# Kernel optimization log

Measured on AMD Instinct MI355X. Metric: run time of the kernel, lower is better.

## Reference

```python
import jax, jax.numpy as jnp
import numpy as np

B, R, NB, T = 32, 96, 5, 2048
FEAT_DIM = 64
SPARSITY = 0.2


def _per_band(X, community, W1, b1, W2, b2):
    # X: [R, T] wavelet coeffs for one (batch, band) slice
    n, t = X.shape
    f32 = X.dtype
    # --- functional connectivity (cosine of centered signals == Pearson corr) ---
    Xc = X - X.mean(axis=1, keepdims=True)
    norm = jnp.linalg.norm(Xc, axis=1, keepdims=True)
    norm = jnp.where(norm == 0, 1.0, norm)
    C = (Xc @ Xc.T) / (norm * norm.T)
    C = jnp.nan_to_num(C, nan=0.0)
    C = C * (1.0 - jnp.eye(n, dtype=f32))  # zero diagonal
    # --- quantile sparsification over strict lower triangle ---
    ti, tj = np.tril_indices(n, -1)
    thr = jnp.quantile(jnp.abs(C[ti, tj]), 1.0 - SPARSITY)
    A = C * (jnp.abs(C) >= thr).astype(f32)  # graph_type == 'weighted'
    # --- node features (5-dim, averaged over regions) ---
    mean_f = X.mean(axis=1)
    std_f = jnp.std(X, axis=1, ddof=1)  # torch.std is unbiased
    energy_f = (X ** 2).sum(axis=1)
    maxamp_f = jnp.abs(X).max(axis=1)
    ps = jnp.abs(jnp.fft.fft(X, axis=1)) ** 2
    ps = ps[:, : t // 2]
    s = ps.sum(axis=1, keepdims=True)
    s = jnp.where(s == 0, 1.0, s)
    p = ps / s
    ent_f = -(p * jnp.log(p + 1e-10)).sum(axis=1)
    node5 = jnp.stack([mean_f, std_f, energy_f, maxamp_f, ent_f], axis=1).mean(axis=0)
    # --- graph properties (6-dim) on binarized adjacency ---
    Bm = (A != 0).astype(f32)
    ne = Bm.sum() / 2.0
    density = ne / (n * (n - 1) / 2.0)
    deg = Bm.sum(axis=1)
    avg_deg = deg.mean()
    A2 = Bm @ Bm
    tri = (A2 * Bm).sum() / 6.0
    poss = (deg * (deg - 1.0)).sum() / 2.0
    clus = jnp.where(poss > 0, tri / jnp.where(poss > 0, poss, 1.0), 0.0)
    # global efficiency: safe reciprocal (zero where A+I == 0; original would emit inf)
    denom = Bm + jnp.eye(n, dtype=f32)
    eff = jnp.where(denom > 0, 1.0 / jnp.where(denom > 0, denom, 1.0), 0.0).sum() / (n * (n - 1))
    # approximate modularity with fixed 2-community assignment (deterministic)
    m2 = 2.0 * ne
    m2_safe = jnp.where(m2 > 0, m2, 1.0)
    same = (community[:, None] == community[None, :]) & (~jnp.eye(n, dtype=bool))
    expected = jnp.outer(deg, deg) / m2_safe
    mod = jnp.where(m2 > 0, (same * (Bm - expected)).sum() / m2_safe, 0.0)
    props = jnp.stack([ne, density, avg_deg, clus, eff, mod])
    feat11 = jnp.concatenate([node5, props])  # [11]
    # --- feature encoder MLP (dropout is identity at inference) ---
    h = jnp.maximum(feat11 @ W1.T + b1, 0.0)
    return A, h @ W2.T + b2


def _forward(wavelet_coeffs, frequency_bands, community, W1, b1, W2, b2):
    b, r, nb, t = wavelet_coeffs.shape
    Xs = wavelet_coeffs.transpose(0, 2, 1, 3).reshape(b * nb, r, t)  # [B*NB, R, T]
    A, F = jax.vmap(_per_band, in_axes=(0, None, None, None, None, None))(
        Xs, community, W1, b1, W2, b2)
    return A.reshape(b, nb, r, r), F.reshape(b, nb, -1)


def setup_inputs() -> dict:
    key = jax.random.key(0)
    k0, k1, k2, k3, k4 = jax.random.split(key, 5)
    wavelet_coeffs = jax.random.normal(k0, (B, R, NB, T), dtype=jnp.float32)
    frequency_bands = jax.random.uniform(k1, (NB, 2), dtype=jnp.float32)
    community = jax.random.randint(k2, (R,), 0, 2)
    W1 = jax.random.normal(k3, (32, 11), dtype=jnp.float32) * 0.3
    b1 = jnp.zeros((32,), jnp.float32)
    W2 = jax.random.normal(k4, (FEAT_DIM, 32), dtype=jnp.float32) * 0.18
    b2 = jnp.zeros((FEAT_DIM,), jnp.float32)
    return {"wavelet_coeffs": wavelet_coeffs, "frequency_bands": frequency_bands,
            "community": community, "W1": W1, "b1": b1, "W2": W2, "b2": b2}


def reference(wavelet_coeffs, frequency_bands, community, W1, b1, W2, b2):
    return _forward(wavelet_coeffs, frequency_bands, community, W1, b1, W2, b2)
```

## Files before the change

kernel.cpp:

```cpp
#include <hip/hip_runtime.h>
#include <hip/hip_bf16.h>
#include <math.h>
#include <float.h>

#ifndef M_PI
#define M_PI 3.14159265358979323846
#endif

#define NBANDS 160
#define RR 96
#define TT 2048
#define NTRIL 4560
#define A_ELEMS ((size_t)NBANDS * RR * RR)
#define NBIN 16384
#define MAXCAND 512

#define PHI(L) ((L) ^ (((L) >> 5) & 31))

typedef float  f32x4  __attribute__((ext_vector_type(4)));
typedef __bf16 bf16x8 __attribute__((ext_vector_type(8)));
typedef __bf16 bf16x4 __attribute__((ext_vector_type(4)));

__device__ inline double blockReduceSum(double v, double* sred) {
    for (int off = 32; off > 0; off >>= 1) v += __shfl_down(v, off, 64);
    int lane = threadIdx.x & 63, wid = threadIdx.x >> 6;
    if (lane == 0) sred[wid] = v;
    __syncthreads();
    int nw = (blockDim.x + 63) >> 6;
    if (threadIdx.x == 0) {
        double r = sred[0];
        for (int i = 1; i < nw; i++) r += sred[i];
        sred[0] = r;
    }
    __syncthreads();
    double r = sred[0];
    __syncthreads();
    return r;
}

__device__ inline void blockReduceSum4(double v0, double v1, double v2, double v3,
                                       double* sred, double out[4]) {
    for (int off = 32; off > 0; off >>= 1) {
        v0 += __shfl_down(v0, off, 64);
        v1 += __shfl_down(v1, off, 64);
        v2 += __shfl_down(v2, off, 64);
        v3 += __shfl_down(v3, off, 64);
    }
    int lane = threadIdx.x & 63, wid = threadIdx.x >> 6;
    if (lane == 0) {
        sred[wid * 4 + 0] = v0; sred[wid * 4 + 1] = v1;
        sred[wid * 4 + 2] = v2; sred[wid * 4 + 3] = v3;
    }
    __syncthreads();
    if (threadIdx.x < 4) {
        double r = sred[threadIdx.x] + sred[4 + threadIdx.x]
                 + sred[8 + threadIdx.x] + sred[12 + threadIdx.x];
        sred[16 + threadIdx.x] = r;
    }
    __syncthreads();
    out[0] = sred[16]; out[1] = sred[17]; out[2] = sred[18]; out[3] = sred[19];
    __syncthreads();
}

__device__ inline void blockReduceSum2(double v0, double v1,
                                       double* sred, double out[2]) {
    for (int off = 32; off > 0; off >>= 1) {
        v0 += __shfl_down(v0, off, 64);
        v1 += __shfl_down(v1, off, 64);
    }
    int lane = threadIdx.x & 63, wid = threadIdx.x >> 6;
    if (lane == 0) { sred[wid * 2 + 0] = v0; sred[wid * 2 + 1] = v1; }
    __syncthreads();
    if (threadIdx.x < 2) {
        double r = sred[threadIdx.x] + sred[2 + threadIdx.x]
                 + sred[4 + threadIdx.x] + sred[6 + threadIdx.x];
        sred[8 + threadIdx.x] = r;
    }
    __syncthreads();
    out[0] = sred[8]; out[1] = sred[9];
    __syncthreads();
}

__device__ inline void blockReduceMax2(double v0, double v1,
                                       double* sred, double out[2]) {
    for (int off = 32; off > 0; off >>= 1) {
        v0 = fmax(v0, __shfl_down(v0, off, 64));
        v1 = fmax(v1, __shfl_down(v1, off, 64));
    }
    int lane = threadIdx.x & 63, wid = threadIdx.x >> 6;
    if (lane == 0) { sred[wid * 2 + 0] = v0; sred[wid * 2 + 1] = v1; }
    __syncthreads();
    if (threadIdx.x < 2) {
        double r = fmax(fmax(sred[threadIdx.x], sred[2 + threadIdx.x]),
                        fmax(sred[4 + threadIdx.x], sred[6 + threadIdx.x]));
        sred[8 + threadIdx.x] = r;
    }
    __syncthreads();
    out[0] = sred[8]; out[1] = sred[9];
    __syncthreads();
}

__global__ void twiddle_kernel(float* tw) {
    int k = blockIdx.x * blockDim.x + threadIdx.x;
    if (k < 1024) {
        double ang = -2.0 * M_PI * (double)k / 2048.0;
        tw[2 * k]     = (float)cos(ang);
        tw[2 * k + 1] = (float)sin(ang);
    }
}

#define BFLY(r1, r2, WR, WI) do { \
    float _wr = (WR), _wi = (WI); \
    float _tr = _wr * yr[r2] - _wi * yi[r2]; \
    float _ti = _wr * yi[r2] + _wi * yr[r2]; \
    yr[r2] = yr[r1] - _tr; yi[r2] = yi[r1] - _ti; \
    yr[r1] += _tr; yi[r1] += _ti; } while (0)

__global__ __launch_bounds__(256) void rowstat_fft_kernel(
    const float* __restrict__ wc, const float* __restrict__ tw,
    double* __restrict__ rowstats)
{
    __shared__ float re[TT];
    __shared__ float im[TT];
    __shared__ double sred[24];
    __shared__ float bcast[4];

    int t = threadIdx.x;
    int g0 = blockIdx.x * 2;
    int g1 = g0 + 1;

    int band = g0 / RR, r0 = g0 % RR;
    int b = band / 5, nb = band % 5;
    size_t base0 = ((size_t)(b * RR + r0) * 5 + nb) * TT;
    size_t base1 = base0 + (size_t)5 * TT;

    float s0 = 0.f, s1 = 0.f, q0 = 0.f, q1 = 0.f, m0 = 0.f, m1 = 0.f;
#pragma unroll
    for (int c = 0; c < 8; c++) {
        int i = t + c * 256;
        float af = wc[base0 + i];
        float bf = wc[base1 + i];
        int P = PHI(i);
        re[P] = af; im[P] = bf;
        s0 += af; s1 += bf;
        q0 = fmaf(af, af, q0); q1 = fmaf(bf, bf, q1);
        m0 = fmaxf(m0, fabsf(af)); m1 = fmaxf(m1, fabsf(bf));
    }
    __syncthreads();

    double S4[4], M2[2];
    blockReduceSum4((double)s0, (double)s1, (double)q0, (double)q1, sred, S4);
    blockReduceMax2((double)m0, (double)m1, sred, M2);
    double SUM0 = S4[0], SUM1 = S4[1], SQ0 = S4[2], SQ1 = S4[3];
    double MX0 = M2[0], MX1 = M2[1];

    float yr[8], yi[8];

#pragma unroll
    for (int j = 0; j < 8; j++) {
        int p = 8 * t + j;
        int L = (int)(__brev((unsigned)p) >> 21);
        int P = PHI(L);
        yr[j] = re[P]; yi[j] = im[P];
    }

    const float RC = 0.70710678f;
    BFLY(0, 1, 1.0f, 0.0f); BFLY(2, 3, 1.0f, 0.0f);
    BFLY(4, 5, 1.0f, 0.0f); BFLY(6, 7, 1.0f, 0.0f);
    BFLY(0, 2, 1.0f, 0.0f); BFLY(1, 3, 0.0f, -1.0f);
    BFLY(4, 6, 1.0f, 0.0f); BFLY(5, 7, 0.0f, -1.0f);
    BFLY(0, 4, 1.0f, 0.0f); BFLY(1, 5, RC, -RC);
    BFLY(2, 6, 0.0f, -1.0f); BFLY(3, 7, -RC, -RC);

    __syncthreads();
#pragma unroll
    for (int j = 0; j < 8; j++) {
        int P = PHI(8 * t + j);
        re[P] = yr[j]; im[P] = yi[j];
    }
    __syncthreads();
    int oo = t & 7;
    int bb64 = 4 * ((t >> 3) & 7) + (t >> 6);
#pragma unroll
    for (int k = 0; k < 8; k++) {
        int P = PHI(64 * bb64 + 8 * k + oo);
        yr[k] = re[P]; yi[k] = im[P];
    }

    {
        int k0 = oo << 7;
        float w0r = tw[2 * k0], w0i = tw[2 * k0 + 1];
        BFLY(0, 1, w0r, w0i); BFLY(2, 3, w0r, w0i);
        BFLY(4, 5, w0r, w0i); BFLY(6, 7, w0r, w0i);
        int ka = oo << 6, kb = (oo + 8) << 6;
        float war = tw[2 * ka], wai = tw[2 * ka + 1];
        float wbr = tw[2 * kb], wbi = tw[2 * kb + 1];
        BFLY(0, 2, war, wai); BFLY(1, 3, wbr, wbi);
        BFLY(4, 6, war, wai); BFLY(5, 7, wbr, wbi);
        int kc0 = oo << 5, kc1 = (oo + 8) << 5, kc2 = (oo + 16) << 5, kc3 = (oo + 24) << 5;
        BFLY(0, 4, tw[2 * kc0], tw[2 * kc0 + 1]);
        BFLY(1, 5, tw[2 * kc1], tw[2 * kc1 + 1]);
        BFLY(2, 6, tw[2 * kc2], tw[2 * kc2 + 1]);
        BFLY(3, 7, tw[2 * kc3], tw[2 * kc3 + 1]);
    }

    __syncthreads();
#pragma unroll
    for (int k = 0; k < 8; k++) {
        int P = PHI(64 * bb64 + 8 * k + oo);
        re[P] = yr[k]; im[P] = yi[k];
    }
    __syncthreads();
    int O3 = t & 63, Wq = t >> 6;
#pragma unroll
    for (int s = 0; s < 2; s++) {
        int B3 = Wq + 4 * s;
#pragma unroll
        for (int k = 0; k < 4; k++) {
            int P = PHI(256 * B3 + 64 * k + O3);
            yr[4 * s + k] = re[P]; yi[4 * s + k] = im[P];
        }
    }

    {
        int kt = O3 << 4;
        float w0r = tw[2 * kt], w0i = tw[2 * kt + 1];
        int ka = O3 << 3, kb = (O3 + 64) << 3;
        float war = tw[2 * ka], wai = tw[2 * ka + 1];
        float wbr = tw[2 * kb], wbi = tw[2 * kb + 1];
        BFLY(0, 1, w0r, w0i); BFLY(2, 3, w0r, w0i);
        BFLY(4, 5, w0r, w0i); BFLY(6, 7, w0r, w0i);
        BFLY(0, 2, war, wai); BFLY(1, 3, wbr, wbi);
        BFLY(4, 6, war, wai); BFLY(5, 7, wbr, wbi);
    }

    __syncthreads();
#pragma unroll
    for (int s = 0; s < 2; s++) {
        int B3 = Wq + 4 * s;
#pragma unroll
        for (int k = 0; k < 4; k++) {
            int P = PHI(256 * B3 + 64 * k + O3);
            re[P] = yr[4 * s + k]; im[P] = yi[4 * s + k];
        }
    }
    __syncthreads();
#pragma unroll
    for (int k = 0; k < 8; k++) {
        int P = PHI(256 * k + t);
        yr[k] = re[P]; yi[k] = im[P];
    }

    {
        int k9 = t << 2;
        float w0r = tw[2 * k9], w0i = tw[2 * k9 + 1];
        BFLY(0, 1, w0r, w0i); BFLY(2, 3, w0r, w0i);
        BFLY(4, 5, w0r, w0i); BFLY(6, 7, w0r, w0i);
        int ka = t << 1, kb = (t + 256) << 1;
        float war = tw[2 * ka], wai = tw[2 * ka + 1];
        float wbr = tw[2 * kb], wbi = tw[2 * kb + 1];
        BFLY(0, 2, war, wai); BFLY(1, 3, wbr, wbi);
        BFLY(4, 6, war, wai); BFLY(5, 7, wbr, wbi);
        BFLY(0, 4, tw[2 * t], tw[2 * t + 1]);
        BFLY(1, 5, tw[2 * (t + 256)], tw[2 * (t + 256) + 1]);
        BFLY(2, 6, tw[2 * (t + 512)], tw[2 * (t + 512) + 1]);
        BFLY(3, 7, tw[2 * (t + 768)], tw[2 * (t + 768) + 1]);
    }

    __syncthreads();
#pragma unroll
    for (int k = 0; k < 8; k++) {
        int P = PHI(256 * k + t);
        re[P] = yr[k]; im[P] = yi[k];
    }
    __syncthreads();

    float psa[8], psb[8];
#pragma unroll
    for (int k = 0; k < 8; k++) {
        int q = (2048 - t - 256 * k) & 2047;
        int P = PHI(q);
        float prr = re[P], pii = im[P];
        float sr = yr[k] + prr, di = yi[k] - pii;
        float si = yi[k] + pii, dr = yr[k] - prr;
        psa[k] = 0.25f * (sr * sr + di * di);
        psb[k] = 0.25f * (si * si + dr * dr);
    }

    float la = 0.f, lb = 0.f;
#pragma unroll
    for (int k = 0; k < 8; k++) { la += psa[k]; lb += psb[k]; }
    double SS[2];
    blockReduceSum2((double)la, (double)lb, sred, SS);
    double SAall = SS[0], SBall = SS[1];
    if (t == 0) {
        bcast[0] = psa[0]; bcast[1] = psa[4];
        bcast[2] = psb[0]; bcast[3] = psb[4];
    }
    __syncthreads();
    double Sa = 0.5 * (SAall + (double)bcast[0] - (double)bcast[1]);
    double Sb = 0.5 * (SBall + (double)bcast[2] - (double)bcast[3]);
    if (Sa == 0.0) Sa = 1.0;
    if (Sb == 0.0) Sb = 1.0;
    float invSa = (float)(1.0 / Sa), invSb = (float)(1.0 / Sb);

    float ea = 0.f, eb = 0.f;
#pragma unroll
    for (int k = 0; k < 8; k++) {
        float pa = psa[k] * invSa;
        float pb = psb[k] * invSb;
        ea += pa * __logf(pa + 1e-10f);
        eb += pb * __logf(pb + 1e-10f);
    }
    double EE[2];
    blockReduceSum2((double)ea, (double)eb, sred, EE);
    double EAall = EE[0], EBall = EE[1];

    if (t == 0) {
        float pa0 = psa[0] * invSa, pa4 = psa[4] * invSa;
        float pb0 = psb[0] * invSb, pb4 = psb[4] * invSb;
        double TA = 0.5 * (EAall + (double)(pa0 * __logf(pa0 + 1e-10f))
                                 - (double)(pa4 * __logf(pa4 + 1e-10f)));
        double TB = 0.5 * (EBall + (double)(pb0 * __logf(pb0 + 1e-10f))
                                 - (double)(pb4 * __logf(pb4 + 1e-10f)));
        double mean0 = SUM0 / (double)TT;
        double mean1 = SUM1 / (double)TT;
        double nsq0 = SQ0 - (double)TT * mean0 * mean0; if (nsq0 < 0) nsq0 = 0;
        double nsq1 = SQ1 - (double)TT * mean1 * mean1; if (nsq1 < 0) nsq1 = 0;
        double* w0 = rowstats + (size_t)g0 * 6;
        double* w1 = rowstats + (size_t)g1 * 6;
        double n0 = sqrt(nsq0), n1 = sqrt(nsq1);
        w0[0] = mean0; w0[1] = (n0 == 0.0 ? 1.0 : n0); w0[2] = sqrt(nsq0 / 2047.0);
        w0[3] = SQ0;   w0[4] = MX0;                    w0[5] = -TA;
        w1[0] = mean1; w1[1] = (n1 == 0.0 ? 1.0 : n1); w1[2] = sqrt(nsq1 / 2047.0);
        w1[3] = SQ1;   w1[4] = MX1;                    w1[5] = -TB;
    }
}

__global__ void zero_kernel(float4* __restrict__ p, int n4) {
    int i = blockIdx.x * blockDim.x + threadIdx.x;
    if (i < n4) p[i] = make_float4(0.f, 0.f, 0.f, 0.f);
}

#define KS 8
#define CHUNK 256
#define BKS 64
#define GPITCH 72
template <bool USE_PART>
__global__ __launch_bounds__(384) void gram_mfma_kernel(
    const float* __restrict__ wc, float* __restrict__ G)
{
    __shared__ __attribute__((aligned(16))) __bf16 sh_hi[RR][GPITCH];
    __shared__ __attribute__((aligned(16))) __bf16 sh_lo[RR][GPITCH];

    int bid = blockIdx.x;
    int band = bid / KS, chunk = bid % KS;
    int b = band / 5, nb = band % 5;
    size_t bandbase = ((size_t)b * RR * 5 + nb) * TT + (size_t)chunk * CHUNK;

    int t = threadIdx.x;
    int wave = t >> 6, lane = t & 63;
    int m16 = lane & 15, quad = lane >> 4;
    int arow = wave * 16 + m16;

    f32x4 acc[6];
#pragma unroll
    for (int ct = 0; ct < 6; ct++) acc[ct] = (f32x4){0.f, 0.f, 0.f, 0.f};

    for (int stage = 0; stage < CHUNK / BKS; stage++) {
        int k0 = stage * BKS;
#pragma unroll
        for (int i = 0; i < 4; i++) {
            int gid = t + i * 384;
            int row = gid >> 4, c4 = gid & 15;
            float4 v = *(const float4*)(wc + bandbase + (size_t)row * (5 * TT) + k0 + c4 * 4);
            __bf16 h0 = (__bf16)v.x, h1 = (__bf16)v.y, h2 = (__bf16)v.z, h3 = (__bf16)v.w;
            __bf16 l0 = (__bf16)(v.x - (float)h0);
            __bf16 l1 = (__bf16)(v.y - (float)h1);
            __bf16 l2 = (__bf16)(v.z - (float)h2);
            __bf16 l3 = (__bf16)(v.w - (float)h3);
// ... 15 lines not shown
                acc[ct] = __builtin_amdgcn_mfma_f32_16x16x32_bf16(ah, bl, acc[ct], 0, 0, 0);
                acc[ct] = __builtin_amdgcn_mfma_f32_16x16x32_bf16(al, bh, acc[ct], 0, 0, 0);
            }
        }
        __syncthreads();
    }

    if (USE_PART) {
        float* Gp = G + (size_t)bid * (RR * RR);
#pragma unroll
        for (int ct = 0; ct < 6; ct++) {
#pragma unroll
            for (int r = 0; r < 4; r++) {
                int grow = wave * 16 + quad * 4 + r;
                int gcol = ct * 16 + m16;
                Gp[grow * RR + gcol] = acc[ct][r];
            }
        }
    } else {
        float* Gb = G + (size_t)band * (RR * RR);
#pragma unroll
        for (int ct = 0; ct < 6; ct++) {
#pragma unroll
            for (int r = 0; r < 4; r++) {
                int grow = wave * 16 + quad * 4 + r;
                int gcol = ct * 16 + m16;
                atomicAdd(&Gb[grow * RR + gcol], acc[ct][r]);
            }
        }
    }
}

template <bool USE_PART>
__global__ __launch_bounds__(256) void normalize_kernel(
    float* __restrict__ G, const float* __restrict__ Gpart,
    const double* __restrict__ rowstats)
{
    int e = blockIdx.x * 256 + threadIdx.x;
    if (e >= (int)(NBANDS * RR * RR)) return;
    int band = e / (RR * RR);
    int rem = e % (RR * RR);
    int i = rem / RR, j = rem % RR;
    double g;
    if (USE_PART) {
        const float* p = Gpart + (size_t)band * KS * (RR * RR) + rem;
        float acc = 0.f;
#pragma unroll
        for (int c = 0; c < KS; c++) acc += p[(size_t)c * (RR * RR)];
        g = (double)acc;
    } else {
        g = (double)G[e];
    }
    const double* rsi = rowstats + (size_t)(band * RR + i) * 6;
    const double* rsj = rowstats + (size_t)(band * RR + j) * 6;
    double c = (g - (double)TT * rsi[0] * rsj[0]) / (rsi[1] * rsj[1]);
    if (i == j) c = 0.0;
    G[e] = (float)c;
}

__global__ __launch_bounds__(256) void quantile_kernel(
    const float* __restrict__ C, double* __restrict__ thr)
{
    __shared__ int hist[NBIN];
    __shared__ int chunk[256];
    __shared__ float cand[MAXCAND];
    __shared__ int ctrl[4];

    int band = blockIdx.x, t = threadIdx.x;
    const float* Cb = C + (size_t)band * (RR * RR);

    for (int i = t; i < NBIN; i += 256) hist[i] = 0;
    if (t == 0) ctrl[3] = 0;
    __syncthreads();

    for (int idx = t; idx < RR * RR; idx += 256) {
        int i = idx / RR, j = idx % RR;
        if (j < i) {
            float val = fabsf(Cb[idx]);
            int bin = (int)(val * (float)NBIN);
            bin = bin > (NBIN - 1) ? (NBIN - 1) : bin;
            atomicAdd(&hist[bin], 1);
        }
    }
    __syncthreads();

    int cs = 0;
    for (int i = 0; i < 64; i++) cs += hist[t * 64 + i];
    chunk[t] = cs;
    __syncthreads();

    if (t == 0) {
        int r0 = 3647, r1 = 3648;
        int cum = 0, c0 = 0;
        while (c0 < 256 && cum + chunk[c0] <= r0) { cum += chunk[c0]; c0++; }
        int bin = c0 * 64, cb = cum;
        while (cb + hist[bin] <= r0) { cb += hist[bin]; bin++; }
        int B0 = bin, cumB0 = cb;
        int bin1 = bin, cb1 = cb;
        while (cb1 + hist[bin1] <= r1) { cb1 += hist[bin1]; bin1++; }
        ctrl[0] = B0; ctrl[1] = bin1; ctrl[2] = cumB0;
    }
    __syncthreads();

    int B0 = ctrl[0], B1 = ctrl[1];
    for (int idx = t; idx < RR * RR; idx += 256) {
        int i = idx / RR, j = idx % RR;
        if (j < i) {
            float val = fabsf(Cb[idx]);
            int bin = (int)(val * (float)NBIN);
            bin = bin > (NBIN - 1) ? (NBIN - 1) : bin;
            if (bin >= B0 && bin <= B1) {
                int k = atomicAdd(&ctrl[3], 1);
                if (k < MAXCAND) cand[k] = val;
            }
        }
    }
    __syncthreads();

    if (t == 0) {
        int n = ctrl[3]; if (n > MAXCAND) n = MAXCAND;
        for (int i = 1; i < n; i++) {
            float key = cand[i]; int j = i - 1;
            while (j >= 0 && cand[j] > key) { cand[j + 1] = cand[j]; j--; }
            cand[j + 1] = key;
        }
        int r0 = 3647 - ctrl[2];
        int r1 = 3648 - ctrl[2];
        double v0 = (double)cand[r0], v1 = (double)cand[r1];
        thr[band] = v0 + 0.2 * (v1 - v0);
    }
}

__global__ __launch_bounds__(256) void graph_feat_kernel(
    const double* __restrict__ thrA,
    const double* __restrict__ rowstats, const int* __restrict__ community,
    const float* __restrict__ W1, const float* __restrict__ b1,
    const float* __restrict__ W2, const float* __restrict__ b2,
    float* __restrict__ A_out, float* __restrict__ F_out)
{
    __shared__ unsigned char Bm[RR][RR];
    __shared__ unsigned long long msk[RR][2];
    __shared__ int deg[RR];
    __shared__ double sred[8];
    __shared__ double feat[11];
    __shared__ double h[32];

    int band = blockIdx.x, t = threadIdx.x;
    double thr = thrA[band];
    float* Ab = A_out + (size_t)band * (RR * RR);

    for (int idx = t; idx < RR * RR; idx += 256) {
        float c = Ab[idx];
        bool keep = ((double)fabsf(c) >= thr);
        Bm[idx / RR][idx % RR] = (keep && c != 0.0f) ? 1 : 0;
        Ab[idx] = keep ? c : 0.0f;
    }
    __syncthreads();

    if (t < RR) {
        unsigned long long m0 = 0, m1 = 0; int d = 0;
        for (int j = 0; j < RR; j++) {
            if (Bm[t][j]) { d++; if (j < 64) m0 |= (1ull << j); else m1 |= (1ull << (j - 64)); }
        }
        msk[t][0] = m0; msk[t][1] = m1; deg[t] = d;
    }
    __syncthreads();

    double triord = 0, ein = 0, expin = 0;
    for (int idx = t; idx < RR * RR; idx += 256) {
        int i = idx / RR, j = idx % RR;
        if (Bm[i][j])
            triord += (double)(__popcll(msk[i][0] & msk[j][0]) +
                               __popcll(msk[i][1] & msk[j][1]));
        if (i != j && community[i] == community[j]) {
            ein += (double)Bm[i][j];
            expin += (double)deg[i] * (double)deg[j];
        }
    }
    double TRI   = blockReduceSum(triord, sred);
    double EIN   = blockReduceSum(ein, sred);
    double EXPIN = blockReduceSum(expin, sred);
    double dv = (t < RR) ? (double)deg[t] : 0.0;
    double DEGS = blockReduceSum(dv, sred);
    double POSS2 = blockReduceSum((t < RR) ? dv * (dv - 1.0) : 0.0, sred);

    const double* rs = rowstats + (size_t)band * RR * 6;
    double N0 = blockReduceSum((t < RR) ? rs[t * 6 + 0] : 0.0, sred);
    double N1 = blockReduceSum((t < RR) ? rs[t * 6 + 2] : 0.0, sred);
    double N2 = blockReduceSum((t < RR) ? rs[t * 6 + 3] : 0.0, sred);
    double N3 = blockReduceSum((t < RR) ? rs[t * 6 + 4] : 0.0, sred);
    double N4 = blockReduceSum((t < RR) ? rs[t * 6 + 5] : 0.0, sred);

    if (t == 0) {
        double ne = 0.5 * DEGS;
        feat[0] = N0 / (double)RR;
        feat[1] = N1 / (double)RR;
        feat[2] = N2 / (double)RR;
        feat[3] = N3 / (double)RR;
        feat[4] = N4 / (double)RR;
        feat[5] = ne;
        feat[6] = ne / (double)NTRIL;
        feat[7] = DEGS / (double)RR;
        double tri = TRI / 6.0, poss = POSS2 * 0.5;
        feat[8] = (poss > 0.0) ? tri / poss : 0.0;
        feat[9] = ((double)RR + DEGS) / ((double)RR * (double)(RR - 1));
        double m2 = DEGS;
        feat[10] = (m2 > 0.0) ? (EIN - EXPIN / m2) / m2 : 0.0;
    }
    __syncthreads();

    if (t < 32) {
        double a = (double)b1[t];
        for (int k = 0; k < 11; k++) a += (double)W1[t * 11 + k] * feat[k];
        h[t] = (a > 0.0) ? a : 0.0;
    }
    __syncthreads();
    if (t < 64) {
        double a = (double)b2[t];
        for (int j = 0; j < 32; j++) a += (double)W2[t * 32 + j] * h[j];
        F_out[(size_t)band * 64 + t] = (float)a;
    }
}

extern "C" void kernel_launch(void* const* d_in, const int* in_sizes, int n_in,
                              void* d_out, int out_size, void* d_ws, size_t ws_size,
                              hipStream_t stream) {
    const float* wc        = (const float*)d_in[0];
    const int*   community = (const int*)d_in[2];
    const float* W1        = (const float*)d_in[3];
    const float* b1        = (const float*)d_in[4];
    const float* W2        = (const float*)d_in[5];
    const float* b2        = (const float*)d_in[6];

    float* A_out = (float*)d_out;
    float* F_out = A_out + A_ELEMS;

    char* ws = (char*)d_ws;
    float*  tw       = (float*)ws;
    double* rowstats = (double*)(ws + 8192);
    double* thr      = (double*)(ws + 745472);
    const size_t PART_OFF   = 747520;
    const size_t PART_BYTES = (size_t)NBANDS * KS * RR * RR * sizeof(float);
    float* Gpart = (float*)(ws + PART_OFF);
    bool use_part = (ws_size >= PART_OFF + PART_BYTES);

    hipLaunchKernelGGL(twiddle_kernel, dim3(4), dim3(256), 0, stream, tw);
    hipLaunchKernelGGL(rowstat_fft_kernel, dim3(NBANDS * RR / 2), dim3(256), 0, stream,
                       wc, tw, rowstats);
    if (use_part) {
        hipLaunchKernelGGL(HIP_KERNEL_NAME(gram_mfma_kernel<true>),
                           dim3(NBANDS * KS), dim3(384), 0, stream, wc, Gpart);
        hipLaunchKernelGGL(HIP_KERNEL_NAME(normalize_kernel<true>),
                           dim3((int)((NBANDS * RR * RR + 255) / 256)), dim3(256), 0, stream,
                           A_out, Gpart, rowstats);
    } else {
        int n4 = (int)(A_ELEMS / 4);
        hipLaunchKernelGGL(zero_kernel, dim3((n4 + 255) / 256), dim3(256), 0, stream,
                           (float4*)A_out, n4);
        hipLaunchKernelGGL(HIP_KERNEL_NAME(gram_mfma_kernel<false>),
                           dim3(NBANDS * KS), dim3(384), 0, stream, wc, A_out);
        hipLaunchKernelGGL(HIP_KERNEL_NAME(normalize_kernel<false>),
                           dim3((int)((NBANDS * RR * RR + 255) / 256)), dim3(256), 0, stream,
                           A_out, A_out, rowstats);
    }
    hipLaunchKernelGGL(quantile_kernel, dim3(NBANDS), dim3(256), 0, stream, A_out, thr);
    hipLaunchKernelGGL(graph_feat_kernel, dim3(NBANDS), dim3(256), 0, stream,
                       thr, rowstats, community, W1, b1, W2, b2, A_out, F_out);
}
```

Measured before the change: 323.0 us.

## Fuse normalize, quantile and graph-feature kernels; process four rows per FFT block

Merges the normalize, quantile and graph-feature kernels into a single per-band finalize kernel. It holds the correlation matrix in shared memory, so A is no longer written and re-read through global memory several times, and two launches are dropped. The FFT kernel now handles four rows per block as two packed complex FFTs, which halves its grid and uses vector twiddle loads. The many serial block reductions are also batched into 4-wide reductions. The cost is more shared memory and registers per block, and fewer blocks available to run in parallel.

```diff
diff --git a/kernel.cpp b/kernel.cpp
--- a/kernel.cpp
+++ b/kernel.cpp
@@ -15,28 +15,16 @@
 #define NBIN 16384
 #define MAXCAND 512
 
+#define KS 8
+#define CHUNK 256
+#define BKS 64
+#define GPITCH 72
+
 #define PHI(L) ((L) ^ (((L) >> 5) & 31))
 
 typedef float  f32x4  __attribute__((ext_vector_type(4)));
 typedef __bf16 bf16x8 __attribute__((ext_vector_type(8)));
 typedef __bf16 bf16x4 __attribute__((ext_vector_type(4)));
-
-__device__ inline double blockReduceSum(double v, double* sred) {
-    for (int off = 32; off > 0; off >>= 1) v += __shfl_down(v, off, 64);
-    int lane = threadIdx.x & 63, wid = threadIdx.x >> 6;
-    if (lane == 0) sred[wid] = v;
-    __syncthreads();
-    int nw = (blockDim.x + 63) >> 6;
-    if (threadIdx.x == 0) {
-        double r = sred[0];
-        for (int i = 1; i < nw; i++) r += sred[i];
-        sred[0] = r;
-    }
-    __syncthreads();
-    double r = sred[0];
-    __syncthreads();
-    return r;
-}
 
 __device__ inline void blockReduceSum4(double v0, double v1, double v2, double v3,
                                        double* sred, double out[4]) {
@@ -81,22 +69,27 @@
     __syncthreads();
 }
 
-__device__ inline void blockReduceMax2(double v0, double v1,
-                                       double* sred, double out[2]) {
+__device__ inline void blockReduceMax4(double v0, double v1, double v2, double v3,
+                                       double* sred, double out[4]) {
     for (int off = 32; off > 0; off >>= 1) {
         v0 = fmax(v0, __shfl_down(v0, off, 64));
         v1 = fmax(v1, __shfl_down(v1, off, 64));
+        v2 = fmax(v2, __shfl_down(v2, off, 64));
+        v3 = fmax(v3, __shfl_down(v3, off, 64));
     }
     int lane = threadIdx.x & 63, wid = threadIdx.x >> 6;
-    if (lane == 0) { sred[wid * 2 + 0] = v0; sred[wid * 2 + 1] = v1; }
-    __syncthreads();
-    if (threadIdx.x < 2) {
-        double r = fmax(fmax(sred[threadIdx.x], sred[2 + threadIdx.x]),
-                        fmax(sred[4 + threadIdx.x], sred[6 + threadIdx.x]));
-        sred[8 + threadIdx.x] = r;
-    }
-    __syncthreads();
-    out[0] = sred[8]; out[1] = sred[9];
+    if (lane == 0) {
+        sred[wid * 4 + 0] = v0; sred[wid * 4 + 1] = v1;
+        sred[wid * 4 + 2] = v2; sred[wid * 4 + 3] = v3;
+    }
+    __syncthreads();
+    if (threadIdx.x < 4) {
+        double r = fmax(fmax(sred[threadIdx.x], sred[4 + threadIdx.x]),
+                        fmax(sred[8 + threadIdx.x], sred[12 + threadIdx.x]));
+        sred[16 + threadIdx.x] = r;
+    }
+    __syncthreads();
+    out[0] = sred[16]; out[1] = sred[17]; out[2] = sred[18]; out[3] = sred[19];
     __syncthreads();
 }
 
@@ -109,74 +102,95 @@
     }
 }
 
-#define BFLY(r1, r2, WR, WI) do { \
+#define BFLYD(r1, r2, WR, WI) do { \
     float _wr = (WR), _wi = (WI); \
-    float _tr = _wr * yr[r2] - _wi * yi[r2]; \
-    float _ti = _wr * yi[r2] + _wi * yr[r2]; \
-    yr[r2] = yr[r1] - _tr; yi[r2] = yi[r1] - _ti; \
-    yr[r1] += _tr; yi[r1] += _ti; } while (0)
+    float _t1r = _wr * yr1[r2] - _wi * yi1[r2]; \
+    float _t1i = _wr * yi1[r2] + _wi * yr1[r2]; \
+    yr1[r2] = yr1[r1] - _t1r; yi1[r2] = yi1[r1] - _t1i; \
+    yr1[r1] += _t1r; yi1[r1] += _t1i; \
+    float _t2r = _wr * yr2[r2] - _wi * yi2[r2]; \
+    float _t2i = _wr * yi2[r2] + _wi * yr2[r2]; \
+    yr2[r2] = yr2[r1] - _t2r; yi2[r2] = yi2[r1] - _t2i; \
+    yr2[r1] += _t2r; yi2[r1] += _t2i; } while (0)
 
 __global__ __launch_bounds__(256) void rowstat_fft_kernel(
     const float* __restrict__ wc, const float* __restrict__ tw,
     double* __restrict__ rowstats)
 {
-    __shared__ float re[TT];
-    __shared__ float im[TT];
+    __shared__ float re1[TT];
+    __shared__ float im1[TT];
+    __shared__ float re2[TT];
+    __shared__ float im2[TT];
     __shared__ double sred[24];
-    __shared__ float bcast[4];
+    __shared__ double statout[12];
+    __shared__ float bcast[8];
 
     int t = threadIdx.x;
-    int g0 = blockIdx.x * 2;
-    int g1 = g0 + 1;
+    int g0 = blockIdx.x * 4;
 
     int band = g0 / RR, r0 = g0 % RR;
     int b = band / 5, nb = band % 5;
     size_t base0 = ((size_t)(b * RR + r0) * 5 + nb) * TT;
-    size_t base1 = base0 + (size_t)5 * TT;
-
-    float s0 = 0.f, s1 = 0.f, q0 = 0.f, q1 = 0.f, m0 = 0.f, m1 = 0.f;
+    const size_t RSTR = (size_t)5 * TT;
+    const float2* twv = (const float2*)tw;
+
+    float s0 = 0.f, s1 = 0.f, s2 = 0.f, s3 = 0.f;
+    float q0 = 0.f, q1 = 0.f, q2 = 0.f, q3 = 0.f;
+    float m0 = 0.f, m1 = 0.f, m2 = 0.f, m3 = 0.f;
 #pragma unroll
     for (int c = 0; c < 8; c++) {
         int i = t + c * 256;
-        float af = wc[base0 + i];
-        float bf = wc[base1 + i];
+        float a0 = wc[base0 + i];
+        float a1 = wc[base0 + RSTR + i];
+        float a2 = wc[base0 + 2 * RSTR + i];
+        float a3 = wc[base0 + 3 * RSTR + i];
         int P = PHI(i);
-        re[P] = af; im[P] = bf;
-        s0 += af; s1 += bf;
-        q0 = fmaf(af, af, q0); q1 = fmaf(bf, bf, q1);
-        m0 = fmaxf(m0, fabsf(af)); m1 = fmaxf(m1, fabsf(bf));
-    }
-    __syncthreads();
-
-    double S4[4], M2[2];
-    blockReduceSum4((double)s0, (double)s1, (double)q0, (double)q1, sred, S4);
-    blockReduceMax2((double)m0, (double)m1, sred, M2);
-    double SUM0 = S4[0], SUM1 = S4[1], SQ0 = S4[2], SQ1 = S4[3];
-    double MX0 = M2[0], MX1 = M2[1];
-
-    float yr[8], yi[8];
+        re1[P] = a0; im1[P] = a1; re2[P] = a2; im2[P] = a3;
+        s0 += a0; s1 += a1; s2 += a2; s3 += a3;
+        q0 = fmaf(a0, a0, q0); q1 = fmaf(a1, a1, q1);
+        q2 = fmaf(a2, a2, q2); q3 = fmaf(a3, a3, q3);
+        m0 = fmaxf(m0, fabsf(a0)); m1 = fmaxf(m1, fabsf(a1));
+        m2 = fmaxf(m2, fabsf(a2)); m3 = fmaxf(m3, fabsf(a3));
+    }
+    __syncthreads();
+
+    {
+        double S[4], Q[4], M[4];
+        blockReduceSum4((double)s0, (double)s1, (double)s2, (double)s3, sred, S);
+        blockReduceSum4((double)q0, (double)q1, (double)q2, (double)q3, sred, Q);
+        blockReduceMax4((double)m0, (double)m1, (double)m2, (double)m3, sred, M);
+        if (t == 0) {
+            statout[0] = S[0]; statout[1] = S[1]; statout[2] = S[2]; statout[3] = S[3];
+            statout[4] = Q[0]; statout[5] = Q[1]; statout[6] = Q[2]; statout[7] = Q[3];
+            statout[8] = M[0]; statout[9] = M[1]; statout[10] = M[2]; statout[11] = M[3];
+        }
+    }
+
+    float yr1[8], yi1[8], yr2[8], yi2[8];
 
 #pragma unroll
     for (int j = 0; j < 8; j++) {
         int p = 8 * t + j;
         int L = (int)(__brev((unsigned)p) >> 21);
         int P = PHI(L);
-        yr[j] = re[P]; yi[j] = im[P];
+        yr1[j] = re1[P]; yi1[j] = im1[P];
+        yr2[j] = re2[P]; yi2[j] = im2[P];
     }
 
     const float RC = 0.70710678f;
-    BFLY(0, 1, 1.0f, 0.0f); BFLY(2, 3, 1.0f, 0.0f);
-    BFLY(4, 5, 1.0f, 0.0f); BFLY(6, 7, 1.0f, 0.0f);
-    BFLY(0, 2, 1.0f, 0.0f); BFLY(1, 3, 0.0f, -1.0f);
-    BFLY(4, 6, 1.0f, 0.0f); BFLY(5, 7, 0.0f, -1.0f);
-    BFLY(0, 4, 1.0f, 0.0f); BFLY(1, 5, RC, -RC);
-    BFLY(2, 6, 0.0f, -1.0f); BFLY(3, 7, -RC, -RC);
+    BFLYD(0, 1, 1.0f, 0.0f); BFLYD(2, 3, 1.0f, 0.0f);
+    BFLYD(4, 5, 1.0f, 0.0f); BFLYD(6, 7, 1.0f, 0.0f);
+    BFLYD(0, 2, 1.0f, 0.0f); BFLYD(1, 3, 0.0f, -1.0f);
+    BFLYD(4, 6, 1.0f, 0.0f); BFLYD(5, 7, 0.0f, -1.0f);
+    BFLYD(0, 4, 1.0f, 0.0f); BFLYD(1, 5, RC, -RC);
+    BFLYD(2, 6, 0.0f, -1.0f); BFLYD(3, 7, -RC, -RC);
 
     __syncthreads();
 #pragma unroll
     for (int j = 0; j < 8; j++) {
         int P = PHI(8 * t + j);
-        re[P] = yr[j]; im[P] = yi[j];
+        re1[P] = yr1[j]; im1[P] = yi1[j];
+        re2[P] = yr2[j]; im2[P] = yi2[j];
     }
     __syncthreads();
     int oo = t & 7;
@@ -184,31 +198,32 @@
 #pragma unroll
     for (int k = 0; k < 8; k++) {
         int P = PHI(64 * bb64 + 8 * k + oo);
-        yr[k] = re[P]; yi[k] = im[P];
+        yr1[k] = re1[P]; yi1[k] = im1[P];
+        yr2[k] = re2[P]; yi2[k] = im2[P];
     }
 
     {
-        int k0 = oo << 7;
-        float w0r = tw[2 * k0], w0i = tw[2 * k0 + 1];
-        BFLY(0, 1, w0r, w0i); BFLY(2, 3, w0r, w0i);
-        BFLY(4, 5, w0r, w0i); BFLY(6, 7, w0r, w0i);
-        int ka = oo << 6, kb = (oo + 8) << 6;
-        float war = tw[2 * ka], wai = tw[2 * ka + 1];
-        float wbr = tw[2 * kb], wbi = tw[2 * kb + 1];
-        BFLY(0, 2, war, wai); BFLY(1, 3, wbr, wbi);
-        BFLY(4, 6, war, wai); BFLY(5, 7, wbr, wbi);
-        int kc0 = oo << 5, kc1 = (oo + 8) << 5, kc2 = (oo + 16) << 5, kc3 = (oo + 24) << 5;
-        BFLY(0, 4, tw[2 * kc0], tw[2 * kc0 + 1]);
-        BFLY(1, 5, tw[2 * kc1], tw[2 * kc1 + 1]);
-        BFLY(2, 6, tw[2 * kc2], tw[2 * kc2 + 1]);
-        BFLY(3, 7, tw[2 * kc3], tw[2 * kc3 + 1]);
+        float2 w0 = twv[oo << 7];
+        BFLYD(0, 1, w0.x, w0.y); BFLYD(2, 3, w0.x, w0.y);
+        BFLYD(4, 5, w0.x, w0.y); BFLYD(6, 7, w0.x, w0.y);
+        float2 wa = twv[oo << 6];
+        float2 wb = twv[(oo + 8) << 6];
+        BFLYD(0, 2, wa.x, wa.y); BFLYD(1, 3, wb.x, wb.y);
+        BFLYD(4, 6, wa.x, wa.y); BFLYD(5, 7, wb.x, wb.y);
+        float2 wc0 = twv[oo << 5], wc1 = twv[(oo + 8) << 5];
+        float2 wc2 = twv[(oo + 16) << 5], wc3 = twv[(oo + 24) << 5];
+        BFLYD(0, 4, wc0.x, wc0.y);
+        BFLYD(1, 5, wc1.x, wc1.y);
+        BFLYD(2, 6, wc2.x, wc2.y);
+        BFLYD(3, 7, wc3.x, wc3.y);
     }
 
     __syncthreads();
 #pragma unroll
     for (int k = 0; k < 8; k++) {
         int P = PHI(64 * bb64 + 8 * k + oo);
-        re[P] = yr[k]; im[P] = yi[k];
+        re1[P] = yr1[k]; im1[P] = yi1[k];
+        re2[P] = yr2[k]; im2[P] = yi2[k];
     }
     __syncthreads();
     int O3 = t & 63, Wq = t >> 6;
@@ -218,20 +233,19 @@
 #pragma unroll
         for (int k = 0; k < 4; k++) {
             int P = PHI(256 * B3 + 64 * k + O3);
-            yr[4 * s + k] = re[P]; yi[4 * s + k] = im[P];
+            yr1[4 * s + k] = re1[P]; yi1[4 * s + k] = im1[P];
+            yr2[4 * s + k] = re2[P]; yi2[4 * s + k] = im2[P];
         }
     }
 
     {
-        int kt = O3 << 4;
-        float w0r = tw[2 * kt], w0i = tw[2 * kt + 1];
-        int ka = O3 << 3, kb = (O3 + 64) << 3;
-        float war = tw[2 * ka], wai = tw[2 * ka + 1];
-        float wbr = tw[2 * kb], wbi = tw[2 * kb + 1];
-        BFLY(0, 1, w0r, w0i); BFLY(2, 3, w0r, w0i);
-        BFLY(4, 5, w0r, w0i); BFLY(6, 7, w0r, w0i);
-        BFLY(0, 2, war, wai); BFLY(1, 3, wbr, wbi);
-        BFLY(4, 6, war, wai); BFLY(5, 7, wbr, wbi);
+        float2 w0 = twv[O3 << 4];
+        float2 wa = twv[O3 << 3];
+        float2 wb = twv[(O3 + 64) << 3];
+        BFLYD(0, 1, w0.x, w0.y); BFLYD(2, 3, w0.x, w0.y);
+        BFLYD(4, 5, w0.x, w0.y); BFLYD(6, 7, w0.x, w0.y);
+        BFLYD(0, 2, wa.x, wa.y); BFLYD(1, 3, wb.x, wb.y);
+        BFLYD(4, 6, wa.x, wa.y); BFLYD(5, 7, wb.x, wb.y);
     }
 
     __syncthreads();
@@ -241,99 +255,124 @@
 #pragma unroll
         for (int k = 0; k < 4; k++) {
             int P = PHI(256 * B3 + 64 * k + O3);
-            re[P] = yr[4 * s + k]; im[P] = yi[4 * s + k];
+            re1[P] = yr1[4 * s + k]; im1[P] = yi1[4 * s + k];
+            re2[P] = yr2[4 * s + k]; im2[P] = yi2[4 * s + k];
         }
     }
     __syncthreads();
 #pragma unroll
     for (int k = 0; k < 8; k++) {
         int P = PHI(256 * k + t);
-        yr[k] = re[P]; yi[k] = im[P];
+        yr1[k] = re1[P]; yi1[k] = im1[P];
+        yr2[k] = re2[P]; yi2[k] = im2[P];
     }
 
     {
-        int k9 = t << 2;
-        float w0r = tw[2 * k9], w0i = tw[2 * k9 + 1];
-        BFLY(0, 1, w0r, w0i); BFLY(2, 3, w0r, w0i);
-        BFLY(4, 5, w0r, w0i); BFLY(6, 7, w0r, w0i);
-        int ka = t << 1, kb = (t + 256) << 1;
-        float war = tw[2 * ka], wai = tw[2 * ka + 1];
-        float wbr = tw[2 * kb], wbi = tw[2 * kb + 1];
-        BFLY(0, 2, war, wai); BFLY(1, 3, wbr, wbi);
-        BFLY(4, 6, war, wai); BFLY(5, 7, wbr, wbi);
-        BFLY(0, 4, tw[2 * t], tw[2 * t + 1]);
-        BFLY(1, 5, tw[2 * (t + 256)], tw[2 * (t + 256) + 1]);
-        BFLY(2, 6, tw[2 * (t + 512)], tw[2 * (t + 512) + 1]);
-        BFLY(3, 7, tw[2 * (t + 768)], tw[2 * (t + 768) + 1]);
+        float2 w0 = twv[t << 2];
+        float2 wa = twv[t << 1];
+        float2 wb = twv[(t + 256) << 1];
+        BFLYD(0, 1, w0.x, w0.y); BFLYD(2, 3, w0.x, w0.y);
+        BFLYD(4, 5, w0.x, w0.y); BFLYD(6, 7, w0.x, w0.y);
+        BFLYD(0, 2, wa.x, wa.y); BFLYD(1, 3, wb.x, wb.y);
+        BFLYD(4, 6, wa.x, wa.y); BFLYD(5, 7, wb.x, wb.y);
+        float2 wf0 = twv[t], wf1 = twv[t + 256];
+        float2 wf2 = twv[t + 512], wf3 = twv[t + 768];
+        BFLYD(0, 4, wf0.x, wf0.y);
+        BFLYD(1, 5, wf1.x, wf1.y);
+        BFLYD(2, 6, wf2.x, wf2.y);
+        BFLYD(3, 7, wf3.x, wf3.y);
     }
 
     __syncthreads();
 #pragma unroll
     for (int k = 0; k < 8; k++) {
         int P = PHI(256 * k + t);
-        re[P] = yr[k]; im[P] = yi[k];
-    }
-    __syncthreads();
-
-    float psa[8], psb[8];
+        re1[P] = yr1[k]; im1[P] = yi1[k];
+        re2[P] = yr2[k]; im2[P] = yi2[k];
+    }
+    __syncthreads();
+
+    float psa1[8], psb1[8], psa2[8], psb2[8];
 #pragma unroll
     for (int k = 0; k < 8; k++) {
         int q = (2048 - t - 256 * k) & 2047;
         int P = PHI(q);
-        float prr = re[P], pii = im[P];
-        float sr = yr[k] + prr, di = yi[k] - pii;
-        float si = yi[k] + pii, dr = yr[k] - prr;
-        psa[k] = 0.25f * (sr * sr + di * di);
-        psb[k] = 0.25f * (si * si + dr * dr);
-    }
-
-    float la = 0.f, lb = 0.f;
-#pragma unroll
-    for (int k = 0; k < 8; k++) { la += psa[k]; lb += psb[k]; }
-    double SS[2];
-    blockReduceSum2((double)la, (double)lb, sred, SS);
-    double SAall = SS[0], SBall = SS[1];
+        float prr = re1[P], pii = im1[P];
+        float sr = yr1[k] + prr, di = yi1[k] - pii;
+        float si = yi1[k] + pii, dr = yr1[k] - prr;
+        psa1[k] = 0.25f * (sr * sr + di * di);
+        psb1[k] = 0.25f * (si * si + dr * dr);
+        float prr2 = re2[P], pii2 = im2[P];
+        float sr2 = yr2[k] + prr2, di2 = yi2[k] - pii2;
+        float si2 = yi2[k] + pii2, dr2 = yr2[k] - prr2;
+        psa2[k] = 0.25f * (sr2 * sr2 + di2 * di2);
+        psb2[k] = 0.25f * (si2 * si2 + dr2 * dr2);
+    }
+
+    float la = 0.f, lb = 0.f, lc = 0.f, ld = 0.f;
+#pragma unroll
+    for (int k = 0; k < 8; k++) {
+        la += psa1[k]; lb += psb1[k]; lc += psa2[k]; ld += psb2[k];
+    }
+    double SS[4];
+    blockReduceSum4((double)la, (double)lb, (double)lc, (double)ld, sred, SS);
     if (t == 0) {
-        bcast[0] = psa[0]; bcast[1] = psa[4];
-        bcast[2] = psb[0]; bcast[3] = psb[4];
-    }
-    __syncthreads();
-    double Sa = 0.5 * (SAall + (double)bcast[0] - (double)bcast[1]);
-    double Sb = 0.5 * (SBall + (double)bcast[2] - (double)bcast[3]);
+        bcast[0] = psa1[0]; bcast[1] = psa1[4];
+        bcast[2] = psb1[0]; bcast[3] = psb1[4];
+        bcast[4] = psa2[0]; bcast[5] = psa2[4];
+        bcast[6] = psb2[0]; bcast[7] = psb2[4];
+    }
+    __syncthreads();
+    double Sa = 0.5 * (SS[0] + (double)bcast[0] - (double)bcast[1]);
+    double Sb = 0.5 * (SS[1] + (double)bcast[2] - (double)bcast[3]);
+    double Sc = 0.5 * (SS[2] + (double)bcast[4] - (double)bcast[5]);
+    double Sd = 0.5 * (SS[3] + (double)bcast[6] - (double)bcast[7]);
     if (Sa == 0.0) Sa = 1.0;
     if (Sb == 0.0) Sb = 1.0;
+    if (Sc == 0.0) Sc = 1.0;
+    if (Sd == 0.0) Sd = 1.0;
     float invSa = (float)(1.0 / Sa), invSb = (float)(1.0 / Sb);
-
-    float ea = 0.f, eb = 0.f;
+    float invSc = (float)(1.0 / Sc), invSd = (float)(1.0 / Sd);
+
+    float ea = 0.f, eb = 0.f, ec = 0.f, ed = 0.f;
 #pragma unroll
     for (int k = 0; k < 8; k++) {
-        float pa = psa[k] * invSa;
-        float pb = psb[k] * invSb;
+        float pa = psa1[k] * invSa;
+        float pb = psb1[k] * invSb;
+        float pc = psa2[k] * invSc;
+        float pd = psb2[k] * invSd;
         ea += pa * __logf(pa + 1e-10f);
         eb += pb * __logf(pb + 1e-10f);
-    }
-    double EE[2];
-    blockReduceSum2((double)ea, (double)eb, sred, EE);
-    double EAall = EE[0], EBall = EE[1];
+        ec += pc * __logf(pc + 1e-10f);
+        ed += pd * __logf(pd + 1e-10f);
+    }
+    double EE[4];
+    blockReduceSum4((double)ea, (double)eb, (double)ec, (double)ed, sred, EE);
 
     if (t == 0) {
-        float pa0 = psa[0] * invSa, pa4 = psa[4] * invSa;
-        float pb0 = psb[0] * invSb, pb4 = psb[4] * invSb;
-        double TA = 0.5 * (EAall + (double)(pa0 * __logf(pa0 + 1e-10f))
+        float pa0 = psa1[0] * invSa, pa4 = psa1[4] * invSa;
+        float pb0 = psb1[0] * invSb, pb4 = psb1[4] * invSb;
+        float pc0 = psa2[0] * invSc, pc4 = psa2[4] * invSc;
+        float pd0 = psb2[0] * invSd, pd4 = psb2[4] * invSd;
+        double TA = 0.5 * (EE[0] + (double)(pa0 * __logf(pa0 + 1e-10f))
                                  - (double)(pa4 * __logf(pa4 + 1e-10f)));
-        double TB = 0.5 * (EBall + (double)(pb0 * __logf(pb0 + 1e-10f))
+        double TB = 0.5 * (EE[1] + (double)(pb0 * __logf(pb0 + 1e-10f))
                                  - (double)(pb4 * __logf(pb4 + 1e-10f)));
-        double mean0 = SUM0 / (double)TT;
-        double mean1 = SUM1 / (double)TT;
-        double nsq0 = SQ0 - (double)TT * mean0 * mean0; if (nsq0 < 0) nsq0 = 0;
-        double nsq1 = SQ1 - (double)TT * mean1 * mean1; if (nsq1 < 0) nsq1 = 0;
-        double* w0 = rowstats + (size_t)g0 * 6;
-        double* w1 = rowstats + (size_t)g1 * 6;
-        double n0 = sqrt(nsq0), n1 = sqrt(nsq1);
-        w0[0] = mean0; w0[1] = (n0 == 0.0 ? 1.0 : n0); w0[2] = sqrt(nsq0 / 2047.0);
-        w0[3] = SQ0;   w0[4] = MX0;                    w0[5] = -TA;
-        w1[0] = mean1; w1[1] = (n1 == 0.0 ? 1.0 : n1); w1[2] = sqrt(nsq1 / 2047.0);
-        w1[3] = SQ1;   w1[4] = MX1;                    w1[5] = -TB;
+        double TC = 0.5 * (EE[2] + (double)(pc0 * __logf(pc0 + 1e-10f))
+                                 - (double)(pc4 * __logf(pc4 + 1e-10f)));
+        double TD = 0.5 * (EE[3] + (double)(pd0 * __logf(pd0 + 1e-10f))
+                                 - (double)(pd4 * __logf(pd4 + 1e-10f)));
+        double TAs[4] = {TA, TB, TC, TD};
+#pragma unroll
+        for (int rix = 0; rix < 4; rix++) {
+            double SUM = statout[rix], SQ = statout[4 + rix], MX = statout[8 + rix];
+            double mean = SUM / (double)TT;
+            double nsq = SQ - (double)TT * mean * mean; if (nsq < 0) nsq = 0;
+            double nrm = sqrt(nsq);
+            double* w = rowstats + (size_t)(g0 + rix) * 6;
+            w[0] = mean; w[1] = (nrm == 0.0 ? 1.0 : nrm); w[2] = sqrt(nsq / 2047.0);
+            w[3] = SQ;   w[4] = MX;                       w[5] = -TAs[rix];
+        }
     }
 }
 
@@ -342,10 +381,6 @@
     if (i < n4) p[i] = make_float4(0.f, 0.f, 0.f, 0.f);
 }
 
-#define KS 8
-#define CHUNK 256
-#define BKS 64
-#define GPITCH 72
 template <bool USE_PART>
 __global__ __launch_bounds__(384) void gram_mfma_kernel(
     const float* __restrict__ wc, float* __restrict__ G)
@@ -427,51 +462,56 @@
 }
 
 template <bool USE_PART>
-__global__ __launch_bounds__(256) void normalize_kernel(
-    float* __restrict__ G, const float* __restrict__ Gpart,
-    const double* __restrict__ rowstats)
+__global__ __launch_bounds__(256) void band_finalize_kernel(
+    const float* __restrict__ Gsrc, const double* __restrict__ rowstats,
+    const int* __restrict__ community,
+    const float* __restrict__ W1, const float* __restrict__ b1,
+    const float* __restrict__ W2, const float* __restrict__ b2,
+    float* __restrict__ A_out, float* __restrict__ F_out)
 {
-    int e = blockIdx.x * 256 + threadIdx.x;
-    if (e >= (int)(NBANDS * RR * RR)) return;
-    int band = e / (RR * RR);
-    int rem = e % (RR * RR);
-    int i = rem / RR, j = rem % RR;
-    double g;
-    if (USE_PART) {
-        const float* p = Gpart + (size_t)band * KS * (RR * RR) + rem;
-        float acc = 0.f;
-#pragma unroll
-        for (int c = 0; c < KS; c++) acc += p[(size_t)c * (RR * RR)];
-        g = (double)acc;
-    } else {
-        g = (double)G[e];
-    }
-    const double* rsi = rowstats + (size_t)(band * RR + i) * 6;
-    const double* rsj = rowstats + (size_t)(band * RR + j) * 6;
-    double c = (g - (double)TT * rsi[0] * rsj[0]) / (rsi[1] * rsj[1]);
-    if (i == j) c = 0.0;
-    G[e] = (float)c;
-}
-
-__global__ __launch_bounds__(256) void quantile_kernel(
-    const float* __restrict__ C, double* __restrict__ thr)
-{
+    __shared__ float Cs[RR][RR];
     __shared__ int hist[NBIN];
-    __shared__ int chunk[256];
+    __shared__ int chunkv[256];
     __shared__ float cand[MAXCAND];
     __shared__ int ctrl[4];
+    __shared__ double mean_s[RR], nrm_s[RR];
+    __shared__ int comm_s[RR];
+    __shared__ unsigned long long msk[RR][2];
+    __shared__ int deg[RR];
+    __shared__ double sred[24];
+    __shared__ double feat[11];
+    __shared__ double hmlp[32];
+    __shared__ double thr_s;
 
     int band = blockIdx.x, t = threadIdx.x;
-    const float* Cb = C + (size_t)band * (RR * RR);
-
+    const double* rsb = rowstats + (size_t)band * RR * 6;
+    if (t < RR) {
+        mean_s[t] = rsb[t * 6 + 0];
+        nrm_s[t]  = rsb[t * 6 + 1];
+        comm_s[t] = community[t];
+    }
     for (int i = t; i < NBIN; i += 256) hist[i] = 0;
     if (t == 0) ctrl[3] = 0;
     __syncthreads();
 
     for (int idx = t; idx < RR * RR; idx += 256) {
         int i = idx / RR, j = idx % RR;
+        float g;
+        if (USE_PART) {
+            const float* p = Gsrc + (size_t)band * KS * (RR * RR) + idx;
+            float acc = 0.f;
+#pragma unroll
+            for (int c = 0; c < KS; c++) acc += p[(size_t)c * (RR * RR)];
+            g = acc;
+        } else {
+            g = Gsrc[(size_t)band * (RR * RR) + idx];
+        }
+        double cd = ((double)g - (double)TT * mean_s[i] * mean_s[j]) / (nrm_s[i] * nrm_s[j]);
+        if (i == j) cd = 0.0;
+        float cf = (float)cd;
+        Cs[i][j] = cf;
         if (j < i) {
-            float val = fabsf(Cb[idx]);
+            float val = fabsf(cf);
             int bin = (int)(val * (float)NBIN);
             bin = bin > (NBIN - 1) ? (NBIN - 1) : bin;
             atomicAdd(&hist[bin], 1);
@@ -481,13 +521,13 @@
 
     int cs = 0;
     for (int i = 0; i < 64; i++) cs += hist[t * 64 + i];
-    chunk[t] = cs;
+    chunkv[t] = cs;
     __syncthreads();
 
     if (t == 0) {
         int r0 = 3647, r1 = 3648;
         int cum = 0, c0 = 0;
-        while (c0 < 256 && cum + chunk[c0] <= r0) { cum += chunk[c0]; c0++; }
+        while (c0 < 256 && cum + chunkv[c0] <= r0) { cum += chunkv[c0]; c0++; }
         int bin = c0 * 64, cb = cum;
         while (cb + hist[bin] <= r0) { cb += hist[bin]; bin++; }
         int B0 = bin, cumB0 = cb;
@@ -501,7 +541,7 @@
     for (int idx = t; idx < RR * RR; idx += 256) {
         int i = idx / RR, j = idx % RR;
         if (j < i) {
-            float val = fabsf(Cb[idx]);
+            float val = fabsf(Cs[i][j]);
             int bin = (int)(val * (float)NBIN);
             bin = bin > (NBIN - 1) ? (NBIN - 1) : bin;
             if (bin >= B0 && bin <= B1) {
@@ -522,69 +562,58 @@
         int r0 = 3647 - ctrl[2];
         int r1 = 3648 - ctrl[2];
         double v0 = (double)cand[r0], v1 = (double)cand[r1];
-        thr[band] = v0 + 0.2 * (v1 - v0);
-    }
-}
-
-__global__ __launch_bounds__(256) void graph_feat_kernel(
-    const double* __restrict__ thrA,
-    const double* __restrict__ rowstats, const int* __restrict__ community,
-    const float* __restrict__ W1, const float* __restrict__ b1,
-    const float* __restrict__ W2, const float* __restrict__ b2,
-    float* __restrict__ A_out, float* __restrict__ F_out)
-{
-    __shared__ unsigned char Bm[RR][RR];
-    __shared__ unsigned long long msk[RR][2];
-    __shared__ int deg[RR];
-    __shared__ double sred[8];
-    __shared__ double feat[11];
-    __shared__ double h[32];
-
-    int band = blockIdx.x, t = threadIdx.x;
-    double thr = thrA[band];
+        thr_s = v0 + 0.2 * (v1 - v0);
+    }
+    __syncthreads();
+    double thr = thr_s;
+
     float* Ab = A_out + (size_t)band * (RR * RR);
-
     for (int idx = t; idx < RR * RR; idx += 256) {
-        float c = Ab[idx];
-        bool keep = ((double)fabsf(c) >= thr);
-        Bm[idx / RR][idx % RR] = (keep && c != 0.0f) ? 1 : 0;
-        Ab[idx] = keep ? c : 0.0f;
-    }
-    __syncthreads();
-
-    if (t < RR) {
-        unsigned long long m0 = 0, m1 = 0; int d = 0;
-        for (int j = 0; j < RR; j++) {
-            if (Bm[t][j]) { d++; if (j < 64) m0 |= (1ull << j); else m1 |= (1ull << (j - 64)); }
-        }
-        msk[t][0] = m0; msk[t][1] = m1; deg[t] = d;
+        float cf = Cs[idx / RR][idx % RR];
+        bool keep = ((double)fabsf(cf) >= thr);
+        Ab[idx] = keep ? cf : 0.f;
+    }
+
+    int lane = t & 63, wid = t >> 6;
+    for (int i = wid; i < RR; i += 4) {
+        float vlo = Cs[i][lane];
+        bool klo = ((double)fabsf(vlo) >= thr) && (vlo != 0.f);
+        unsigned long long blo = __ballot(klo);
+        float vhi = Cs[i][64 + (lane & 31)];
+        bool khi = (lane < 32) && ((double)fabsf(vhi) >= thr) && (vhi != 0.f);
+        unsigned long long bhi = __ballot(khi) & 0xffffffffull;
+        if (lane == 0) {
+            msk[i][0] = blo; msk[i][1] = bhi;
+            deg[i] = __popcll(blo) + __popcll(bhi);
+        }
     }
     __syncthreads();
 
     double triord = 0, ein = 0, expin = 0;
     for (int idx = t; idx < RR * RR; idx += 256) {
         int i = idx / RR, j = idx % RR;
-        if (Bm[i][j])
-            triord += (double)(__popcll(msk[i][0] & msk[j][0]) +
-                               __popcll(msk[i][1] & msk[j][1]));
-        if (i != j && community[i] == community[j]) {
-            ein += (double)Bm[i][j];
+        unsigned long long mi0 = msk[i][0], mi1 = msk[i][1];
+        bool bij = (((j < 64) ? (mi0 >> j) : (mi1 >> (j - 64))) & 1ull) != 0;
+        if (bij)
+            triord += (double)(__popcll(mi0 & msk[j][0]) +
+                               __popcll(mi1 & msk[j][1]));
+        if (i != j && comm_s[i] == comm_s[j]) {
+            ein += bij ? 1.0 : 0.0;
             expin += (double)deg[i] * (double)deg[j];
         }
     }
-    double TRI   = blockReduceSum(triord, sred);
-    double EIN   = blockReduceSum(ein, sred);
-    double EXPIN = blockReduceSum(expin, sred);
     double dv = (t < RR) ? (double)deg[t] : 0.0;
-    double DEGS = blockReduceSum(dv, sred);
-    double POSS2 = blockReduceSum((t < RR) ? dv * (dv - 1.0) : 0.0, sred);
-
-    const double* rs = rowstats + (size_t)band * RR * 6;
-    double N0 = blockReduceSum((t < RR) ? rs[t * 6 + 0] : 0.0, sred);
-    double N1 = blockReduceSum((t < RR) ? rs[t * 6 + 2] : 0.0, sred);
-    double N2 = blockReduceSum((t < RR) ? rs[t * 6 + 3] : 0.0, sred);
-    double N3 = blockReduceSum((t < RR) ? rs[t * 6 + 4] : 0.0, sred);
-    double N4 = blockReduceSum((t < RR) ? rs[t * 6 + 5] : 0.0, sred);
+    double R1[4], R2[4], R3[2];
+    blockReduceSum4(triord, ein, expin, dv, sred, R1);
+    blockReduceSum4((t < RR) ? dv * (dv - 1.0) : 0.0,
+                    (t < RR) ? rsb[t * 6 + 0] : 0.0,
+                    (t < RR) ? rsb[t * 6 + 2] : 0.0,
+                    (t < RR) ? rsb[t * 6 + 3] : 0.0, sred, R2);
+    blockReduceSum2((t < RR) ? rsb[t * 6 + 4] : 0.0,
+                    (t < RR) ? rsb[t * 6 + 5] : 0.0, sred, R3);
+    double TRI = R1[0], EIN = R1[1], EXPIN = R1[2], DEGS = R1[3];
+    double POSS2 = R2[0], N0 = R2[1], N1 = R2[2], N2 = R2[3];
+    double N3 = R3[0], N4 = R3[1];
 
     if (t == 0) {
         double ne = 0.5 * DEGS;
@@ -607,12 +636,12 @@
     if (t < 32) {
         double a = (double)b1[t];
         for (int k = 0; k < 11; k++) a += (double)W1[t * 11 + k] * feat[k];
-        h[t] = (a > 0.0) ? a : 0.0;
+        hmlp[t] = (a > 0.0) ? a : 0.0;
     }
     __syncthreads();
     if (t < 64) {
         double a = (double)b2[t];
-        for (int j = 0; j < 32; j++) a += (double)W2[t * 32 + j] * h[j];
+        for (int j = 0; j < 32; j++) a += (double)W2[t * 32 + j] * hmlp[j];
         F_out[(size_t)band * 64 + t] = (float)a;
     }
 }
@@ -633,32 +662,28 @@
     char* ws = (char*)d_ws;
     float*  tw       = (float*)ws;
     double* rowstats = (double*)(ws + 8192);
-    double* thr      = (double*)(ws + 745472);
     const size_t PART_OFF   = 747520;
     const size_t PART_BYTES = (size_t)NBANDS * KS * RR * RR * sizeof(float);
     float* Gpart = (float*)(ws + PART_OFF);
     bool use_part = (ws_size >= PART_OFF + PART_BYTES);
 
     hipLaunchKernelGGL(twiddle_kernel, dim3(4), dim3(256), 0, stream, tw);
-    hipLaunchKernelGGL(rowstat_fft_kernel, dim3(NBANDS * RR / 2), dim3(256), 0, stream,
+    hipLaunchKernelGGL(rowstat_fft_kernel, dim3(NBANDS * RR / 4), dim3(256), 0, stream,
                        wc, tw, rowstats);
     if (use_part) {
         hipLaunchKernelGGL(HIP_KERNEL_NAME(gram_mfma_kernel<true>),
                            dim3(NBANDS * KS), dim3(384), 0, stream, wc, Gpart);
-        hipLaunchKernelGGL(HIP_KERNEL_NAME(normalize_kernel<true>),
-                           dim3((int)((NBANDS * RR * RR + 255) / 256)), dim3(256), 0, stream,
-                           A_out, Gpart, rowstats);
+        hipLaunchKernelGGL(HIP_KERNEL_NAME(band_finalize_kernel<true>),
+                           dim3(NBANDS), dim3(256), 0, stream,
+                           Gpart, rowstats, community, W1, b1, W2, b2, A_out, F_out);
     } else {
         int n4 = (int)(A_ELEMS / 4);
         hipLaunchKernelGGL(zero_kernel, dim3((n4 + 255) / 256), dim3(256), 0, stream,
                            (float4*)A_out, n4);
         hipLaunchKernelGGL(HIP_KERNEL_NAME(gram_mfma_kernel<false>),
                            dim3(NBANDS * KS), dim3(384), 0, stream, wc, A_out);
-        hipLaunchKernelGGL(HIP_KERNEL_NAME(normalize_kernel<false>),
-                           dim3((int)((NBANDS * RR * RR + 255) / 256)), dim3(256), 0, stream,
-                           A_out, A_out, rowstats);
-    }
-    hipLaunchKernelGGL(quantile_kernel, dim3(NBANDS), dim3(256), 0, stream, A_out, thr);
-    hipLaunchKernelGGL(graph_feat_kernel, dim3(NBANDS), dim3(256), 0, stream,
-                       thr, rowstats, community, W1, b1, W2, b2, A_out, F_out);
-}
+        hipLaunchKernelGGL(HIP_KERNEL_NAME(band_finalize_kernel<false>),
+                           dim3(NBANDS), dim3(256), 0, stream,
+                           A_out, rowstats, community, W1, b1, W2, b2, A_out, F_out);
+    }
+}
```

Result: faster. 309.7 us (-4.1%).
